# Performance work log

Measured on AMD Instinct MI355X. Metric: run time of the kernel, lower is better.

## Reference

```python
import jax, jax.numpy as jnp
import numpy as np

DIM = 768
HEADS = 12
HEAD_DIM = DIM // HEADS
R = 8            # LoRA rank (cfg.EXPERT_LOW_RANK)
E = 4            # number of routed LoRA experts in proj (cfg.EXPERT_NUM)
LORA_SCALE = 1.0 / R   # lora_alpha(=1) / r
TOPK_T_PCT = 50  # cfg.topk_tempalte (percent)
TOPK_S_PCT = 25  # cfg.topk_search (percent)
B = 4
N_M = 256        # template / memory tokens
N_S = 1024       # search tokens
N = N_M + N_S
MEM = 1280       # cached memory kv length


def setup_inputs() -> dict:
    key = jax.random.key(0)
    ks = jax.random.split(key, 24)
    g = lambda i, shape: jax.random.normal(ks[i], shape, dtype=jnp.float32) * 0.02
    return dict(
        x=jax.random.normal(ks[0], (B, N, DIM), dtype=jnp.float32),
        id_total=jax.random.normal(ks[1], (B, N_M, DIM), dtype=jnp.float32),
        mem_k=jax.random.normal(ks[2], (B, HEADS, MEM, HEAD_DIM), dtype=jnp.float32),
        mem_v=jax.random.normal(ks[3], (B, HEADS, MEM, HEAD_DIM), dtype=jnp.float32),
        W_qkv=g(4, (3 * DIM, DIM)), b_qkv=g(5, (3 * DIM,)),
        qkv_A=g(6, (3, R, DIM)), qkv_B=g(7, (3, DIM, R)),
        W_proj=g(8, (DIM, DIM)), b_proj=g(9, (DIM,)),
        route_W=g(10, (E, DIM)), proj_A=g(11, (E, R, DIM)), proj_B=g(12, (E, DIM, R)),
        W_idk=g(13, (HEADS, DIM)), b_idk=g(14, (HEADS,)),
        idk_A=g(15, (R, DIM)), idk_B=g(16, (HEADS, R)),
        W_idv=g(17, (DIM, DIM)), b_idv=g(18, (DIM,)),
        idv_A=g(19, (R, DIM)), idv_B=g(20, (DIM, R)),
    )


def _lora1(x, W, b, A, Bm):
    # LinearExperts with lora_num=1: softmax over a single route logit == 1.0
    return x @ W.T + b + ((x @ A.T) @ Bm.T) * LORA_SCALE


def _softmax_w_top(att, top):
    # topk values (sorted desc) -> stable exp relative to the max -> normalize -> scatter
    vals, idx = jax.lax.top_k(att, top)
    e = jnp.exp(vals - vals[..., :1])
    e = e / jnp.sum(e, axis=-1, keepdims=True)
    b, h, q, _ = att.shape
    bi = jnp.arange(b)[:, None, None, None]
    hi = jnp.arange(h)[None, :, None, None]
    qi = jnp.arange(q)[None, None, :, None]
    return jnp.zeros_like(att).at[bi, hi, qi, idx].set(e.astype(att.dtype))


def _forward(x, id_total, mem_k, mem_v, W_qkv, b_qkv, qkv_A, qkv_B,
             W_proj, b_proj, route_W, proj_A, proj_B,
             W_idk, b_idk, idk_A, idk_B, W_idv, b_idv, idv_A, idv_B):
    Bb, Nn, C = x.shape
    Nm = id_total.shape[1]
    Ns = Nn - Nm
    H, D = HEADS, C // HEADS
    # MergedLinear qkv: dense + per-group (q,k,v) LoRA
    low = jnp.einsum('bnc,grc->bngr', x, qkv_A)
    lora = (jnp.einsum('bngr,gcr->bngc', low, qkv_B) * LORA_SCALE).reshape(Bb, Nn, 3 * C)
    qkv = (x @ W_qkv.T + b_qkv + lora).reshape(Bb, Nn, 3, H, D).transpose(2, 0, 3, 1, 4)
    q, k, v = qkv[0], qkv[1], qkv[2]          # each (B,H,N,D)
    k_m, v_m, v_s = k[:, :, :Nm], v[:, :, :Nm], v[:, :, Nm:]
    # memory-token ID gating (id_add=True path)
    ID_K = _lora1(id_total, W_idk, b_idk, idk_A, idk_B)   # (B,Nm,H)
    ID_V = _lora1(id_total, W_idv, b_idv, idv_A, idv_B)   # (B,Nm,C)
    k_m_id = k_m * (1.0 + jnp.tanh(ID_K)).transpose(0, 2, 1)[..., None]
    v_m_flat = v_m.transpose(0, 2, 1, 3).reshape(Bb, Nm, C) + ID_V
    v_m_id = v_m_flat.reshape(Bb, Nm, H, D).transpose(0, 2, 1, 3)
    v_add_id = jnp.concatenate([v_m_id, v_s], axis=2)
    q = q * (D ** -0.5)
    q_m, q_s = q[:, :, :Nm], q[:, :, Nm:]
    # template self-attention with topk softmax
    attn_m = q_m @ k_m_id.transpose(0, 1, 3, 2)           # (B,H,Nm,Nm)
    attn_m = _softmax_w_top(attn_m, int(TOPK_T_PCT / 100 * Nm))
    x_m = (attn_m @ v_m_id).transpose(0, 2, 1, 3).reshape(Bb, Nm, C)
    # search attention over [mem_k, k] (k is the ORIGINAL un-gated key, as in torch)
    k_full = jnp.concatenate([mem_k, k], axis=2)
    v_full = jnp.concatenate([mem_v, v_add_id], axis=2)
    attn_s = q_s @ k_full.transpose(0, 1, 3, 2)           # (B,H,Ns,MEM+N)
    attn_s = _softmax_w_top(attn_s, int(TOPK_S_PCT / 100 * k_full.shape[2]))
    x_s = (attn_s @ v_full).transpose(0, 2, 1, 3).reshape(Bb, Ns, C)
    xo = jnp.concatenate([x_m, x_s], axis=1)
    # LinearExperts proj: dense + softmax-routed LoRA experts
    route = jax.nn.softmax((xo @ route_W.T).astype(jnp.float32), axis=-1).astype(xo.dtype)
    low = jnp.einsum('bnc,erc->bner', xo, proj_A)
    up = jnp.einsum('bner,ecr->bnec', low, proj_B)
    out = xo @ W_proj.T + b_proj + jnp.einsum('bne,bnec->bnc', route, up) * LORA_SCALE
    return out, k_m_id, v_m_id


def reference(x, id_total, mem_k, mem_v, W_qkv, b_qkv, qkv_A, qkv_B,
              W_proj, b_proj, route_W, proj_A, proj_B,
              W_idk, b_idk, idk_A, idk_B, W_idv, b_idv, idv_A, idv_B):
    return _forward(x, id_total, mem_k, mem_v, W_qkv, b_qkv, qkv_A, qkv_B,
                    W_proj, b_proj, route_W, proj_A, proj_B,
                    W_idk, b_idk, idk_A, idk_B, W_idv, b_idv, idv_A, idv_B)
```

## Files before the change

### kernel.cpp

```cpp
#include <hip/hip_runtime.h>
#include <cstddef>

#define Bq    4
#define Hh    12
#define Dd    64
#define NNtok 1280
#define DIMc  768
#define KAUG  800
#define NBH   48

typedef __attribute__((ext_vector_type(8))) short bf16x8;
typedef __attribute__((ext_vector_type(4))) float f32x4;

static const size_t OVb   = 0;
static const size_t OXO   = 3932160;
static const size_t OQL   = 7864320;
static const size_t OIDK  = 7987200;
static const size_t OIDV  = 7999488;
static const size_t OLK   = 8785920;
static const size_t OLV   = 8794112;
static const size_t ORD   = 8802304;
static const size_t OPL   = 8822784;
static const size_t OQH   = 8986624;
static const size_t OKFH  = 10952704;
static const size_t OVTH  = 14884864;
static const size_t OKMH  = 18817024;
static const size_t OVMTH = 19210240;
static const size_t OAa   = 19603456;
static const size_t OWa   = 21651456;
static const size_t OWa2  = 22573056;

static const size_t KMID_OFF = 3932160;
static const size_t VMID_OFF = 4718592;

__device__ __forceinline__ unsigned int pk_bf16(float a, float b) {
  unsigned int ua = __float_as_uint(a), ub = __float_as_uint(b);
  ua += 0x7fffu + ((ua >> 16) & 1u);
  ub += 0x7fffu + ((ub >> 16) & 1u);
  return (ua >> 16) | (ub & 0xffff0000u);
}
__device__ __forceinline__ unsigned short bf16_1(float a) {
  unsigned int ua = __float_as_uint(a);
  ua += 0x7fffu + ((ua >> 16) & 1u);
  return (unsigned short)(ua >> 16);
}
__device__ __forceinline__ float bf2f(unsigned int h) {
  return __uint_as_float(h << 16);
}

__global__ __launch_bounds__(256) void prep(
    const float* __restrict__ mem_k, const float* __restrict__ mem_v,
    const float* __restrict__ W_qkv, const float* __restrict__ qkvB,
    const float* __restrict__ W_proj, const float* __restrict__ projB,
    unsigned short* __restrict__ kfh, unsigned short* __restrict__ vth,
    unsigned short* __restrict__ Wa, unsigned short* __restrict__ Wa2)
{
  __shared__ float tl[64][65];
  const int blk = blockIdx.x, t = threadIdx.x;
  if (blk < 1920) {
    size_t idx = ((size_t)blk * 256 + t) * 8;
    int bh = (int)(idx / 81920);
    int r  = (int)(idx % 81920);
    const float* s = mem_k + (size_t)bh * 81920 + r;
    float4 a = *(const float4*)s;
    float4 b = *(const float4*)(s + 4);
    unsigned int* dp = (unsigned int*)(kfh + (size_t)bh * 163840 + r);
    dp[0] = pk_bf16(a.x, a.y); dp[1] = pk_bf16(a.z, a.w);
    dp[2] = pk_bf16(b.x, b.y); dp[3] = pk_bf16(b.z, b.w);
  } else if (blk < 2880) {
    int b2 = blk - 1920;
    int bh = b2 / 20, t0 = (b2 % 20) * 64;
    const float* sb = mem_v + (size_t)bh * 81920 + (size_t)t0 * 64;
#pragma unroll
    for (int p = 0; p < 4; ++p) {
      int flat = p * 256 + t;
      int r = flat >> 4, c4 = (flat & 15) << 2;
      float4 v = *(const float4*)(sb + r * 64 + c4);
      tl[r][c4 + 0] = v.x; tl[r][c4 + 1] = v.y;
      tl[r][c4 + 2] = v.z; tl[r][c4 + 3] = v.w;
    }
    __syncthreads();
    unsigned short* db = vth + (size_t)bh * 163840 + t0;
#pragma unroll
    for (int p = 0; p < 8; ++p) {
      int flat = p * 256 + t;
      int d = flat >> 5, u = flat & 31;
      *(unsigned int*)(db + (size_t)d * 2560 + 2 * u) = pk_bf16(tl[2 * u][d], tl[2 * u + 1][d]);
    }
  } else if (blk < 6480) {
    int idx = (blk - 2880) * 256 + t;
    int row = idx / 400, c = (idx % 400) * 2;
    float a, b;
    if (c < 768) {
      a = W_qkv[(size_t)row * 768 + c]; b = W_qkv[(size_t)row * 768 + c + 1];
    } else {
      int g = row / 768, jj = row % 768;
      int e0 = c - 768, e1 = e0 + 1;
      a = (e0 < 24 && (e0 >> 3) == g) ? qkvB[(size_t)g * 6144 + jj * 8 + (e0 & 7)] * 0.125f : 0.f;
      b = (e1 < 24 && (e1 >> 3) == g) ? qkvB[(size_t)g * 6144 + jj * 8 + (e1 & 7)] * 0.125f : 0.f;
    }
    *(unsigned int*)(Wa + (size_t)row * KAUG + c) = pk_bf16(a, b);
  } else {
    int idx = (blk - 6480) * 256 + t;
    int row = idx / 400, c = (idx % 400) * 2;
    float a, b;
    if (c < 768) {
      a = W_proj[(size_t)row * 768 + c]; b = W_proj[(size_t)row * 768 + c + 1];
    } else {
      int e0 = c - 768, e1 = e0 + 1;
      a = projB[(size_t)(e0 >> 3) * 6144 + row * 8 + (e0 & 7)];
      b = projB[(size_t)(e1 >> 3) * 6144 + row * 8 + (e1 & 7)];
    }
    *(unsigned int*)(Wa2 + (size_t)row * KAUG + c) = pk_bf16(a, b);
  }
}

__global__ __launch_bounds__(256) void dot_small(
    const float* __restrict__ src, const float* __restrict__ mat,
    float* __restrict__ dst, int nout)
{
  int wv = threadIdx.x >> 6, ln = threadIdx.x & 63;
  size_t row = (size_t)blockIdx.x * 4 + wv;
  const float* s = src + row * DIMc;
  for (int o = 0; o < nout; ++o) {
    float p = 0.f;
    const float* m = mat + (size_t)o * DIMc;
    for (int c = ln; c < DIMc; c += 64) p += s[c] * m[c];
    for (int off = 32; off; off >>= 1) p += __shfl_xor(p, off, 64);
    if (ln == 0) dst[row * nout + o] = p;
  }
}

__global__ __launch_bounds__(256) void dot_id(
    const float* __restrict__ id_tot, const float* __restrict__ idkA,
    const float* __restrict__ idvA, float* __restrict__ lowk,
    float* __restrict__ lowv)
{
  int wv = threadIdx.x >> 6, ln = threadIdx.x & 63;
  size_t row = (size_t)blockIdx.x * 4 + wv;
  const float* s = id_tot + row * DIMc;
  for (int o = 0; o < 8; ++o) {
    float p = 0.f, q = 0.f;
    const float* m1 = idkA + (size_t)o * DIMc;
    const float* m2 = idvA + (size_t)o * DIMc;
    for (int c = ln; c < DIMc; c += 64) { p += s[c] * m1[c]; q += s[c] * m2[c]; }
    for (int off = 32; off; off >>= 1) { p += __shfl_xor(p, off, 64); q += __shfl_xor(q, off, 64); }
    if (ln == 0) { lowk[row * 8 + o] = p; lowv[row * 8 + o] = q; }
  }
}

__global__ __launch_bounds__(256) void dot_rp(
    const float* __restrict__ xo, const float* __restrict__ routeW,
    const float* __restrict__ projA, float* __restrict__ rd,
    float* __restrict__ plow)
{
  int wv = threadIdx.x >> 6, ln = threadIdx.x & 63;
  size_t row = (size_t)blockIdx.x * 4 + wv;
  const float* s = xo + row * DIMc;
  float xr[12];
#pragma unroll
  for (int i = 0; i < 12; ++i) xr[i] = s[ln + i * 64];
  for (int o = 0; o < 4; ++o) {
    float p = 0.f;
    const float* m = routeW + (size_t)o * DIMc;
#pragma unroll
    for (int i = 0; i < 12; ++i) p += xr[i] * m[ln + i * 64];
    for (int off = 32; off; off >>= 1) p += __shfl_xor(p, off, 64);
    if (ln == 0) rd[row * 4 + o] = p;
  }
  for (int o = 0; o < 32; ++o) {
    float p = 0.f;
    const float* m = projA + (size_t)o * DIMc;
#pragma unroll
    for (int i = 0; i < 12; ++i) p += xr[i] * m[ln + i * 64];
    for (int off = 32; off; off >>= 1) p += __shfl_xor(p, off, 64);
    if (ln == 0) plow[row * 32 + o] = p;
  }
}

__global__ __launch_bounds__(256) void idv_idk(
    const float* __restrict__ id_tot,
    const float* __restrict__ W_idv, const float* __restrict__ b_idv,
    const float* __restrict__ lowv, const float* __restrict__ idv_B,
    float* __restrict__ IDV,
    const float* __restrict__ W_idk, const float* __restrict__ b_idk,
    const float* __restrict__ lowk, const float* __restrict__ idk_B,
    float* __restrict__ IDK)
{
  __shared__ alignas(16) float As[16][68];
  __shared__ alignas(16) float Bs[16][68];
  const int blk = blockIdx.x, t = threadIdx.x;
  if (blk < 192) {
    const int tx = t & 15, ty = t >> 4;
    const int bn = (blk % 12) * 64, bm = (blk / 12) * 64;
    const int am = t >> 2, ak = (t & 3) << 2;
    float acc[4][4] = {};
    for (int k0 = 0; k0 < 768; k0 += 16) {
      float4 av = *(const float4*)(id_tot + (size_t)(bm + am) * 768 + k0 + ak);
      float4 bv = *(const float4*)(W_idv + (size_t)(bn + am) * 768 + k0 + ak);
      As[ak + 0][am] = av.x; As[ak + 1][am] = av.y; As[ak + 2][am] = av.z; As[ak + 3][am] = av.w;
      Bs[ak + 0][am] = bv.x; Bs[ak + 1][am] = bv.y; Bs[ak + 2][am] = bv.z; Bs[ak + 3][am] = bv.w;
      __syncthreads();
#pragma unroll
      for (int kk = 0; kk < 16; ++kk) {
        float4 a4 = *(const float4*)&As[kk][ty << 2];
        float4 b4 = *(const float4*)&Bs[kk][tx << 2];
        float ar[4] = { a4.x, a4.y, a4.z, a4.w };
        float br[4] = { b4.x, b4.y, b4.z, b4.w };
#pragma unroll
        for (int i = 0; i < 4; ++i)
#pragma unroll
          for (int j = 0; j < 4; ++j) acc[i][j] += ar[i] * br[j];
      }
      __syncthreads();
    }
#pragma unroll
    for (int i = 0; i < 4; ++i) {
      int mg = bm + (ty << 2) + i;
#pragma unroll
      for (int j = 0; j < 4; ++j) {
        int col = bn + (tx << 2) + j;
        float v = acc[i][j] + b_idv[col];
        float lo = 0.f;
#pragma unroll
        for (int r = 0; r < 8; ++r) lo += lowv[(size_t)mg * 8 + r] * idv_B[(size_t)col * 8 + r];
        IDV[(size_t)mg * 768 + col] = v + lo * 0.125f;
      }
    }
  } else {
    int wv = t >> 6, ln = t & 63;
    size_t row = (size_t)(blk - 192) * 4 + wv;
    const float* s = id_tot + row * DIMc;
    for (int h = 0; h < Hh; ++h) {
      float p = 0.f;
      const float* m = W_idk + (size_t)h * DIMc;
      for (int c = ln; c < DIMc; c += 64) p += s[c] * m[c];
      for (int off = 32; off; off >>= 1) p += __shfl_xor(p, off, 64);
      if (ln == 0) {
        float lo = 0.f;
        for (int r = 0; r < 8; ++r) lo += lowk[row * 8 + r] * idk_B[h * 8 + r];
        IDK[row * Hh + h] = 1.f + tanhf(p + b_idk[h] + lo * 0.125f);
      }
    }
  }
}

__global__ __launch_bounds__(256) void fixup_kernel(
    float* __restrict__ vb, const float* __restrict__ IDK,
    const float* __restrict__ IDV, float* __restrict__ kmid,
    float* __restrict__ vmid, unsigned short* __restrict__ kmh)
{
  int e = blockIdx.x * 256 + threadIdx.x;
  int d  = e & 63;
  int r1 = e >> 6;
  int tt = r1 & 255;
  int r2 = r1 >> 8;
  int h  = r2 % Hh;
  int b  = r2 / Hh;
  float km = kmid[e] * IDK[(size_t)(b * 256 + tt) * Hh + h];
  kmid[e] = km;
  kmh[e] = bf16_1(km);
  size_t src = ((size_t)(b * Hh + h) * NNtok + tt) * Dd + d;
  float vv = vb[src] + IDV[(size_t)(b * 256 + tt) * DIMc + h * 64 + d];
  vb[src] = vv;
  vmid[e] = vv;
}

__global__ __launch_bounds__(256) void transpose_post(
    const float* __restrict__ vb, unsigned short* __restrict__ vth,
    unsigned short* __restrict__ vmth)
{
  __shared__ float tl[64][65];
  const int blk = blockIdx.x, t = threadIdx.x;
  int bh, t0, dstCols, colOfs;
  unsigned short* dstp;
  size_t dstBh;
  if (blk < 960) { bh = blk / 20; t0 = (blk % 20) * 64; dstp = vth; dstBh = 163840; dstCols = 2560; colOfs = 1280; }
  else { int b2 = blk - 960; bh = b2 / 4; t0 = (b2 % 4) * 64; dstp = vmth; dstBh = 16384; dstCols = 256; colOfs = 0; }
  const float* sb = vb + (size_t)bh * 81920 + (size_t)t0 * 64;
#pragma unroll
  for (int p = 0; p < 4; ++p) {
    int flat = p * 256 + t;
    int r = flat >> 4, c4 = (flat & 15) << 2;
    float4 v = *(const float4*)(sb + r * 64 + c4);
    tl[r][c4 + 0] = v.x; tl[r][c4 + 1] = v.y;
    tl[r][c4 + 2] = v.z; tl[r][c4 + 3] = v.w;
  }
  __syncthreads();
  unsigned short* db = dstp + (size_t)bh * dstBh + colOfs + t0;
#pragma unroll
  for (int p = 0; p < 8; ++p) {
    int flat = p * 256 + t;
    int d = flat >> 5, u = flat & 31;
    *(unsigned int*)(db + (size_t)d * dstCols + 2 * u) = pk_bf16(tl[2 * u][d], tl[2 * u + 1][d]);
  }
}

__global__ __launch_bounds__(256) void cast_pack(
    const float* __restrict__ mainp, const float* __restrict__ extra,
    unsigned short* __restrict__ dst, int extraN)
{
  int idx = blockIdx.x * 256 + threadIdx.x;
  int row = idx / 100, c8 = (idx % 100) * 8;
  unsigned int w[4];
  if (c8 < 768) {
    const float* s = mainp + (size_t)row * 768 + c8;
    float4 a = *(const float4*)s;
    float4 b = *(const float4*)(s + 4);
    w[0] = pk_bf16(a.x, a.y); w[1] = pk_bf16(a.z, a.w);
    w[2] = pk_bf16(b.x, b.y); w[3] = pk_bf16(b.z, b.w);
  } else {
    float v[8];
#pragma unroll
    for (int j = 0; j < 8; ++j) {
      int e = c8 - 768 + j;
      v[j] = (e < extraN) ? extra[(size_t)row * extraN + e] : 0.f;
    }
    w[0] = pk_bf16(v[0], v[1]); w[1] = pk_bf16(v[2], v[3]);
    w[2] = pk_bf16(v[4], v[5]); w[3] = pk_bf16(v[6], v[7]);
  }
  *(uint4*)(dst + (size_t)row * KAUG + c8) = make_uint4(w[0], w[1], w[2], w[3]);
}

__global__ __launch_bounds__(256) void cast_pack_proj(
    const float* __restrict__ xo, const float* __restrict__ rd,
    const float* __restrict__ plow, unsigned short* __restrict__ dst)
{
  int idx = blockIdx.x * 256 + threadIdx.x;
  int row = idx / 100, c8 = (idx % 100) * 8;
  unsigned int w[4];
  if (c8 < 768) {
    const float* s = xo + (size_t)row * 768 + c8;
    float4 a = *(const float4*)s;
    float4 b = *(const float4*)(s + 4);
    w[0] = pk_bf16(a.x, a.y); w[1] = pk_bf16(a.z, a.w);
    w[2] = pk_bf16(b.x, b.y); w[3] = pk_bf16(b.z, b.w);
  } else {
    float l0 = rd[row * 4 + 0], l1 = rd[row * 4 + 1], l2 = rd[row * 4 + 2], l3 = rd[row * 4 + 3];
    float m = fmaxf(fmaxf(l0, l1), fmaxf(l2, l3));
    float e0 = __expf(l0 - m), e1 = __expf(l1 - m), e2 = __expf(l2 - m), e3 = __expf(l3 - m);
    float inv = 0.125f / (e0 + e1 + e2 + e3);
    float rt[4] = { e0 * inv, e1 * inv, e2 * inv, e3 * inv };
    float v[8];
#pragma unroll
    for (int j = 0; j < 8; ++j) {
      int e = c8 - 768 + j;
      v[j] = (e < 32) ? rt[e >> 3] * plow[(size_t)row * 32 + e] : 0.f;
    }
    w[0] = pk_bf16(v[0], v[1]); w[1] = pk_bf16(v[2], v[3]);
    w[2] = pk_bf16(v[4], v[5]); w[3] = pk_bf16(v[6], v[7]);
  }
  *(uint4*)(dst + (size_t)row * KAUG + c8) = make_uint4(w[0], w[1], w[2], w[3]);
}

__global__ __launch_bounds__(256) void gemm_mfma(
    const unsigned short* __restrict__ A, const unsigned short* __restrict__ W,
    const float* __restrict__ bias, int mode, float* __restrict__ dst,
    unsigned short* __restrict__ qh, float* __restrict__ kmid,
    float* __restrict__ vb, unsigned short* __restrict__ kfh)
{
  const int t = threadIdx.x, w = t >> 6, l = t & 63;
  const int m = l & 15, quad = l >> 4;
  const int bm = blockIdx.y * 128 + (w >> 1) * 64;
  const int bn = blockIdx.x * 128 + (w & 1) * 64;
  f32x4 acc[4][4] = {};
  const unsigned short* Ab = A + (size_t)(bm + m) * KAUG;
  const unsigned short* Wb = W + (size_t)(bn + m) * KAUG;
  for (int kk = 0; kk < KAUG; kk += 32) {
    bf16x8 af[4], bf[4];
#pragma unroll
    for (int i = 0; i < 4; ++i) af[i] = *(const bf16x8*)(Ab + (size_t)i * 16 * KAUG + kk + quad * 8);
#pragma unroll
    for (int j = 0; j < 4; ++j) bf[j] = *(const bf16x8*)(Wb + (size_t)j * 16 * KAUG + kk + quad * 8);
#pragma unroll
    for (int i = 0; i < 4; ++i)
#pragma unroll
      for (int j = 0; j < 4; ++j)
        acc[i][j] = __builtin_amdgcn_mfma_f32_16x16x32_bf16(af[i], bf[j], acc[i][j], 0, 0, 0);
  }

  float bj[4];
#pragma unroll
  for (int j = 0; j < 4; ++j) bj[j] = bias[bn + j * 16 + m];

  if (mode == 2) {
#pragma unroll
    for (int i = 0; i < 4; ++i)
#pragma unroll
      for (int r = 0; r < 4; ++r) {
        int row = bm + i * 16 + quad * 4 + r;
#pragma unroll
        for (int j = 0; j < 4; ++j)
          dst[(size_t)row * 768 + bn + j * 16 + m] = acc[i][j][r] + bj[j];
      }
    return;
  }
  int g = (blockIdx.x * 128) / DIMc;
#pragma unroll
  for (int j = 0; j < 4; ++j) {
    int col = bn + j * 16 + m;
    int jj = col - g * DIMc, hh = jj >> 6, d = jj & 63;
#pragma unroll
    for (int i = 0; i < 4; ++i)
#pragma unroll
      for (int r = 0; r < 4; ++r) {
        int row = bm + i * 16 + quad * 4 + r;
        int bb = row / NNtok, tt = row % NNtok;
        float v = acc[i][j][r] + bj[j];
        if (g == 0) {
          qh[((size_t)(bb * Hh + hh) * NNtok + tt) * Dd + d] = bf16_1(v * 0.125f);
        } else if (g == 1) {
          kfh[((size_t)(bb * Hh + hh) * 2560 + 1280 + tt) * Dd + d] = bf16_1(v);
          if (tt < 256) kmid[((size_t)(bb * Hh + hh) * 256 + tt) * Dd + d] = v;
        } else {
          vb[((size_t)(bb * Hh + hh) * NNtok + tt) * Dd + d] = v;
        }
      }
  }
}

__device__ __forceinline__ void radix_sel(
    unsigned int* hist, int l, int& kk, int& ceq, unsigned int& bin)
{
  unsigned int h0 = hist[4 * l + 0], h1 = hist[4 * l + 1],
               h2 = hist[4 * l + 2], h3 = hist[4 * l + 3];
  unsigned int s3 = h3, s2 = h2 + s3, s1 = h1 + s2, s0 = h0 + s1;
  unsigned int tsum = s0;
#pragma unroll
  for (int off = 1; off < 64; off <<= 1) {
    unsigned int other = __shfl(tsum, l + off, 64);
    tsum += (l + off < 64) ? other : 0u;
  }
  unsigned int T = tsum - s0;
  unsigned int Sv0 = T + s0, Sv1 = T + s1, Sv2 = T + s2, Sv3 = T + s3, Sv4 = T;
  int fb = -1, fkk = 0, fceq = 0;
  unsigned int ukk = (unsigned int)kk;
  if (Sv0 >= ukk && Sv1 < ukk) { fb = 4 * l + 0; fkk = (int)(ukk - Sv1); fceq = (int)(Sv0 - Sv1); }
  if (Sv1 >= ukk && Sv2 < ukk) { fb = 4 * l + 1; fkk = (int)(ukk - Sv2); fceq = (int)(Sv1 - Sv2); }
  if (Sv2 >= ukk && Sv3 < ukk) { fb = 4 * l + 2; fkk = (int)(ukk - Sv3); fceq = (int)(Sv2 - Sv3); }
  if (Sv3 >= ukk && Sv4 < ukk) { fb = 4 * l + 3; fkk = (int)(ukk - Sv4); fceq = (int)(Sv3 - Sv4); }
  unsigned long long mb = __ballot(fb >= 0);
  int src = __ffsll(mb) - 1;
  bin = (unsigned int)__shfl(fb, src, 64);
  kk  = __shfl(fkk, src, 64);
  ceq = __shfl(fceq, src, 64);
}

template<int NK>
__global__ __launch_bounds__(256, 3) void attn_mfma7(
    const unsigned short* __restrict__ qh,
    const unsigned short* __restrict__ kf,
    const unsigned short* __restrict__ vt,
    int TK, int qrow0, float* __restrict__ xo, int nofs)
{
  constexpr int SCP = NK + 8;
  constexpr int W = NK / 128;
  constexpr int NRB = (NK == 256) ? 32 : 128;
  __shared__ alignas(16) unsigned short sc16[8][SCP];
  __shared__ unsigned int hist8[8][256];
  __shared__ float wavemax[4][8];
  __shared__ float rowinv[8];

  const int t = threadIdx.x, w = t >> 6, l = t & 63;
  const int xcd  = (int)blockIdx.x & 7;
  const int slot = (int)blockIdx.x >> 3;
  const int bh   = xcd * (NBH / 8) + slot / NRB;
  const int rb   = slot % NRB;
  const int b = bh / Hh, h = bh % Hh;
  const int qbase = qrow0 + rb * 8;
  const int m = l & 15, quad = l >> 4;

  bf16x8 aq0 = {0,0,0,0,0,0,0,0}, aq1 = {0,0,0,0,0,0,0,0};
  if (m < 8) {
    const unsigned short* qp = qh + ((size_t)bh * NNtok + qbase + m) * Dd + quad * 8;
    aq0 = *(const bf16x8*)qp;
    aq1 = *(const bf16x8*)(qp + 32);
  }
  float mx[4] = { -3.0e38f, -3.0e38f, -3.0e38f, -3.0e38f };
  constexpr int ITA = NK / 64;
  constexpr int GA = (ITA >= 4) ? 4 : ITA;
  const unsigned short* kpA = kf + (size_t)bh * NK * Dd + (size_t)(w * 16 + m) * Dd + quad * 8;
  bf16x8 kbuf[2][GA][2];
#pragma unroll
  for (int i = 0; i < GA; ++i) {
    kbuf[0][i][0] = *(const bf16x8*)(kpA + (size_t)i * 64 * Dd);
    kbuf[0][i][1] = *(const bf16x8*)(kpA + (size_t)i * 64 * Dd + 32);
  }
  int ab = 0;
  for (int g0 = 0; g0 < ITA; g0 += GA) {
    if (g0 + GA < ITA) {
#pragma unroll
      for (int i = 0; i < GA; ++i) {
        kbuf[1 - ab][i][0] = *(const bf16x8*)(kpA + (size_t)(g0 + GA + i) * 64 * Dd);
        kbuf[1 - ab][i][1] = *(const bf16x8*)(kpA + (size_t)(g0 + GA + i) * 64 * Dd + 32);
      }
    }
#pragma unroll
    for (int i = 0; i < GA; ++i) {
      int n0 = w * 16 + (g0 + i) * 64;
      f32x4 acc = {0.f, 0.f, 0.f, 0.f};
      acc = __builtin_amdgcn_mfma_f32_16x16x32_bf16(aq0, kbuf[ab][i][0], acc, 0, 0, 0);
      acc = __builtin_amdgcn_mfma_f32_16x16x32_bf16(aq1, kbuf[ab][i][1], acc, 0, 0, 0);
      if (quad < 2) {
#pragma unroll
        for (int r = 0; r < 4; ++r) {
          float v = acc[r];
          mx[r] = fmaxf(mx[r], v);
          sc16[quad * 4 + r][n0 + m] = bf16_1(v);
        }
      }
    }
    ab ^= 1;
  }
#pragma unroll
  for (int off = 1; off < 16; off <<= 1)
#pragma unroll
    for (int r = 0; r < 4; ++r) mx[r] = fmaxf(mx[r], __shfl_xor(mx[r], off, 64));
  if (l == 0) {
#pragma unroll
    for (int r = 0; r < 4; ++r) wavemax[w][r] = mx[r];
  }
  if (l == 16) {
#pragma unroll
    for (int r = 0; r < 4; ++r) wavemax[w][4 + r] = mx[r];
  }
  __syncthreads();

  const int r0i = w * 2, r1i = w * 2 + 1;
  unsigned int* sp0 = (unsigned int*)&sc16[r0i][0];
  unsigned int* sp1 = (unsigned int*)&sc16[r1i][0];
  unsigned int* h0 = hist8[r0i];
  unsigned int* h1 = hist8[r1i];
#pragma unroll
  for (int z = 0; z < 4; ++z) { h0[l + z * 64] = 0u; h1[l + z * 64] = 0u; }
  unsigned int kw0[W], kw1[W];
#pragma unroll
  for (int j = 0; j < W; ++j) {
    unsigned int v0 = sp0[j * 64 + l];
    unsigned int v1 = sp1[j * 64 + l];
    v0 = v0 ^ (((v0 >> 15) & 0x00010001u) * 0x7fffu + 0x80008000u);
    v1 = v1 ^ (((v1 >> 15) & 0x00010001u) * 0x7fffu + 0x80008000u);
    kw0[j] = v0; kw1[j] = v1;
    atomicAdd(&h0[(v0 >> 8) & 255u], 1u);
    atomicAdd(&h0[v0 >> 24], 1u);
    atomicAdd(&h1[(v1 >> 8) & 255u], 1u);
    atomicAdd(&h1[v1 >> 24], 1u);
  }
  int kk0 = TK, kk1 = TK;
  int ceq0s, ceq1s;
  unsigned int bin0, bin1;
  radix_sel(h0, l, kk0, ceq0s, bin0);
  radix_sel(h1, l, kk1, ceq1s, bin1);
  const unsigned int pf0 = bin0 << 8, pf1 = bin1 << 8;
  (void)ceq0s; (void)ceq1s;

  auto finish = [&](unsigned int* kwp, unsigned int prefix, int kk, int row,
                    unsigned int* sp) {
    unsigned int* hist = hist8[row];
#pragma unroll
    for (int z = 0; z < 4; ++z) hist[l + z * 64] = 0u;
    const unsigned int pfx8 = prefix >> 8;
#pragma unroll
    for (int j = 0; j < W; ++j) {
      unsigned int k2 = kwp[j];
      unsigned int lo = k2 & 0xFFFFu, hi = k2 >> 16;
      if ((lo >> 8) == pfx8) atomicAdd(&hist[lo & 255u], 1u);
      if ((hi >> 8) == pfx8) atomicAdd(&hist[hi & 255u], 1u);
    }
    unsigned int b2;
    int ceq = 0;
    radix_sel(hist, l, kk, ceq, b2);
    const unsigned int Tkey = prefix | b2;
    const int need = kk;
    if (need < ceq) {
      int seen = 0;
      unsigned long long below = (1ull << l) - 1ull;
#pragma unroll
      for (int j = 0; j < W; ++j) {
        unsigned int k2 = kwp[j];
        bool eq0 = ((k2 & 0xFFFFu) == Tkey);
        bool eq1 = ((k2 >> 16) == Tkey);
        unsigned long long m0 = __ballot(eq0), m1 = __ballot(eq1);
        int bfr = __popcll(m0 & below) + __popcll(m1 & below);
        if (eq0 && (seen + bfr) >= need) kwp[j] &= 0xFFFF0000u;
        if (eq1 && (seen + bfr + (eq0 ? 1 : 0)) >= need) kwp[j] &= 0x0000FFFFu;
        seen += __popcll(m0) + __popcll(m1);
      }
    }
    float rm = fmaxf(fmaxf(wavemax[0][row], wavemax[1][row]),
                     fmaxf(wavemax[2][row], wavemax[3][row]));
    float sum = 0.f;
#pragma unroll
    for (int j = 0; j < W; ++j) {
      unsigned int k2 = kwp[j];
      unsigned int lo = k2 & 0xFFFFu, hi = k2 >> 16;
      unsigned int mm = ((~k2 >> 15) & 0x00010001u) * 0x7fffu + 0x80008000u;
      unsigned int o2 = k2 ^ mm;
      float v0 = bf2f(o2 & 0xFFFFu);
      float v1 = bf2f(o2 >> 16);
      float w0 = (lo >= Tkey) ? __expf(v0 - rm) : 0.f;
      float w1 = (hi >= Tkey) ? __expf(v1 - rm) : 0.f;
      sp[j * 64 + l] = pk_bf16(w0, w1);
      sum += w0 + w1;
    }
#pragma unroll
    for (int off = 32; off; off >>= 1) sum += __shfl_xor(sum, off, 64);
    if (l == 0) rowinv[row] = 1.f / sum;
  };
  finish(kw0, pf0, kk0, r0i, sp0);
  finish(kw1, pf1, kk1, r1i, sp1);
  __syncthreads();

  constexpr int ITD = NK / 32;
  constexpr int GD = (ITD >= 4) ? 4 : ITD;
  const unsigned short* vrow = vt + (size_t)bh * Dd * NK + (size_t)(w * 16 + m) * NK + quad * 8;
  f32x4 o = {0.f, 0.f, 0.f, 0.f};
  const bf16x8 zz = {0,0,0,0,0,0,0,0};
  bf16x8 vbuf[2][GD], wbuf[2][GD];
#pragma unroll
  for (int i = 0; i < GD; ++i) {
    vbuf[0][i] = *(const bf16x8*)(vrow + i * 32);
    wbuf[0][i] = (m < 8) ? *(const bf16x8*)&sc16[m][i * 32 + quad * 8] : zz;
  }
  int db = 0;
  for (int g0 = 0; g0 < ITD; g0 += GD) {
    if (g0 + GD < ITD) {
#pragma unroll
      for (int i = 0; i < GD; ++i) {
        vbuf[1 - db][i] = *(const bf16x8*)(vrow + (g0 + GD + i) * 32);
        wbuf[1 - db][i] = (m < 8) ? *(const bf16x8*)&sc16[m][(g0 + GD + i) * 32 + quad * 8] : zz;
      }
    }
#pragma unroll
    for (int i = 0; i < GD; ++i)
      o = __builtin_amdgcn_mfma_f32_16x16x32_bf16(wbuf[db][i], vbuf[db][i], o, 0, 0, 0);
    db ^= 1;
  }
  if (quad < 2) {
#pragma unroll
    for (int r = 0; r < 4; ++r) {
      int row = quad * 4 + r;
      int n = nofs + rb * 8 + row;
      xo[((size_t)b * NNtok + n) * DIMc + h * 64 + w * 16 + m] = o[r] * rowinv[row];
    }
  }
}

extern "C" void kernel_launch(void* const* d_in, const int* in_sizes, int n_in,
                              void* d_out, int out_size, void* d_ws, size_t ws_size,
                              hipStream_t stream)
{
  const float* x       = (const float*)d_in[0];
  const float* id_tot  = (const float*)d_in[1];
  const float* mem_k   = (const float*)d_in[2];
  const float* mem_v   = (const float*)d_in[3];
  const float* W_qkv   = (const float*)d_in[4];
  const float* b_qkv   = (const float*)d_in[5];
  const float* qkv_A   = (const float*)d_in[6];
  const float* qkv_B   = (const float*)d_in[7];
  const float* W_proj  = (const float*)d_in[8];
  const float* b_proj  = (const float*)d_in[9];
  const float* route_W = (const float*)d_in[10];
  const float* proj_A  = (const float*)d_in[11];
  const float* proj_B  = (const float*)d_in[12];
  const float* W_idk   = (const float*)d_in[13];
  const float* b_idk   = (const float*)d_in[14];
  const float* idk_A   = (const float*)d_in[15];
  const float* idk_B   = (const float*)d_in[16];
  const float* W_idv   = (const float*)d_in[17];
  const float* b_idv   = (const float*)d_in[18];
  const float* idv_A   = (const float*)d_in[19];
  const float* idv_B   = (const float*)d_in[20];

  float* ws   = (float*)d_ws;
  float* vb   = ws + OVb;
  float* xo   = ws + OXO;
  float* qlow = ws + OQL;
  float* IDK  = ws + OIDK;
  float* IDV  = ws + OIDV;
  float* lowk = ws + OLK;
  float* lowv = ws + OLV;
  float* rd   = ws + ORD;
  float* plow = ws + OPL;
  unsigned short* qh   = (unsigned short*)(ws + OQH);
  unsigned short* kfh  = (unsigned short*)(ws + OKFH);
  unsigned short* vth  = (unsigned short*)(ws + OVTH);
  unsigned short* kmh  = (unsigned short*)(ws + OKMH);
  unsigned short* vmth = (unsigned short*)(ws + OVMTH);
  unsigned short* Aa   = (unsigned short*)(ws + OAa);
  unsigned short* Wa   = (unsigned short*)(ws + OWa);
  unsigned short* Wa2  = (unsigned short*)(ws + OWa2);

  float* out  = (float*)d_out;
  float* kmid = out + KMID_OFF;
  float* vmid = out + VMID_OFF;

  prep<<<7680, 256, 0, stream>>>(mem_k, mem_v, W_qkv, qkv_B, W_proj, proj_B,
                                 kfh, vth, Wa, Wa2);

  dot_small<<<1280, 256, 0, stream>>>(x, qkv_A, qlow, 24);
  dot_id<<<256, 256, 0, stream>>>(id_tot, idk_A, idv_A, lowk, lowv);

  cast_pack<<<2000, 256, 0, stream>>>(x, qlow, Aa, 24);
  gemm_mfma<<<dim3(18, 40), 256, 0, stream>>>(Aa, Wa, b_qkv, 0, nullptr,
                                              qh, kmid, vb, kfh);
  idv_idk<<<448, 256, 0, stream>>>(id_tot, W_idv, b_idv, lowv, idv_B, IDV,
                                   W_idk, b_idk, lowk, idk_B, IDK);
  fixup_kernel<<<3072, 256, 0, stream>>>(vb, IDK, IDV, kmid, vmid, kmh);

  transpose_post<<<1152, 256, 0, stream>>>(vb, vth, vmth);

  attn_mfma7<256><<<1536, 256, 0, stream>>>(qh, kmh, vmth, 128, 0, xo, 0);
  attn_mfma7<2560><<<6144, 256, 0, stream>>>(qh, kfh, vth, 640, 256, xo, 256);

  dot_rp<<<1280, 256, 0, stream>>>(xo, route_W, proj_A, rd, plow);
  cast_pack_proj<<<2000, 256, 0, stream>>>(xo, rd, plow, Aa);
  gemm_mfma<<<dim3(6, 40), 256, 0, stream>>>(Aa, Wa2, b_proj, 2, out,
                                             nullptr, nullptr, nullptr, nullptr);
}
```

Measured before the change: 914.9 us.

## Shrink attention LDS footprint via XOR swizzle and aliased histogram for higher occupancy

Removes the padded score rows, separate histogram, wavemax and rowinv shared arrays. Scores are stored with an XOR swizzle instead of padding to avoid bank conflicts. For large NK the radix histogram now reuses each row's score buffer while keys sit in registers, and the row max comes from the encoded keys via a wave reduction. Launch bounds rise from 3 to 4 blocks per CU, trading two extra barriers and more aliasing complexity for higher occupancy.

After: 1.064 ms. 16.2% more time.

```diff
diff --git a/kernel.cpp b/kernel.cpp
--- a/kernel.cpp
+++ b/kernel.cpp
@@ -447,19 +447,15 @@
 }
 
 template<int NK>
-__global__ __launch_bounds__(256, 3) void attn_mfma7(
+__global__ __launch_bounds__(256, 4) void attn_mfma7(
     const unsigned short* __restrict__ qh,
     const unsigned short* __restrict__ kf,
     const unsigned short* __restrict__ vt,
     int TK, int qrow0, float* __restrict__ xo, int nofs)
 {
-  constexpr int SCP = NK + 8;
   constexpr int W = NK / 128;
   constexpr int NRB = (NK == 256) ? 32 : 128;
-  __shared__ alignas(16) unsigned short sc16[8][SCP];
-  __shared__ unsigned int hist8[8][256];
-  __shared__ float wavemax[4][8];
-  __shared__ float rowinv[8];
+  __shared__ alignas(16) unsigned short sc16[8 * NK];
 
   const int t = threadIdx.x, w = t >> 6, l = t & 63;
   const int xcd  = (int)blockIdx.x & 7;
@@ -476,7 +472,6 @@
     aq0 = *(const bf16x8*)qp;
     aq1 = *(const bf16x8*)(qp + 32);
   }
-  float mx[4] = { -3.0e38f, -3.0e38f, -3.0e38f, -3.0e38f };
   constexpr int ITA = NK / 64;
   constexpr int GA = (ITA >= 4) ? 4 : ITA;
   const unsigned short* kpA = kf + (size_t)bh * NK * Dd + (size_t)(w * 16 + m) * Dd + quad * 8;
@@ -504,73 +499,87 @@
       if (quad < 2) {
 #pragma unroll
         for (int r = 0; r < 4; ++r) {
-          float v = acc[r];
-          mx[r] = fmaxf(mx[r], v);
-          sc16[quad * 4 + r][n0 + m] = bf16_1(v);
+          int row = quad * 4 + r;
+          int s = n0 + m;
+          int dw = (s >> 1) ^ (row << 2);
+          sc16[row * NK + dw * 2 + (s & 1)] = bf16_1(acc[r]);
         }
       }
     }
     ab ^= 1;
   }
-#pragma unroll
-  for (int off = 1; off < 16; off <<= 1)
-#pragma unroll
-    for (int r = 0; r < 4; ++r) mx[r] = fmaxf(mx[r], __shfl_xor(mx[r], off, 64));
-  if (l == 0) {
-#pragma unroll
-    for (int r = 0; r < 4; ++r) wavemax[w][r] = mx[r];
-  }
-  if (l == 16) {
-#pragma unroll
-    for (int r = 0; r < 4; ++r) wavemax[w][4 + r] = mx[r];
-  }
   __syncthreads();
 
   const int r0i = w * 2, r1i = w * 2 + 1;
-  unsigned int* sp0 = (unsigned int*)&sc16[r0i][0];
-  unsigned int* sp1 = (unsigned int*)&sc16[r1i][0];
-  unsigned int* h0 = hist8[r0i];
-  unsigned int* h1 = hist8[r1i];
-#pragma unroll
-  for (int z = 0; z < 4; ++z) { h0[l + z * 64] = 0u; h1[l + z * 64] = 0u; }
+  unsigned int* sp0 = (unsigned int*)&sc16[r0i * NK];
+  unsigned int* sp1 = (unsigned int*)&sc16[r1i * NK];
+  const int sw0 = r0i << 2, sw1 = r1i << 2;
   unsigned int kw0[W], kw1[W];
+  unsigned int km0 = 0u, km1 = 0u;
 #pragma unroll
   for (int j = 0; j < W; ++j) {
-    unsigned int v0 = sp0[j * 64 + l];
-    unsigned int v1 = sp1[j * 64 + l];
+    unsigned int v0 = sp0[(j * 64 + l) ^ sw0];
+    unsigned int v1 = sp1[(j * 64 + l) ^ sw1];
     v0 = v0 ^ (((v0 >> 15) & 0x00010001u) * 0x7fffu + 0x80008000u);
     v1 = v1 ^ (((v1 >> 15) & 0x00010001u) * 0x7fffu + 0x80008000u);
     kw0[j] = v0; kw1[j] = v1;
-    atomicAdd(&h0[(v0 >> 8) & 255u], 1u);
-    atomicAdd(&h0[v0 >> 24], 1u);
-    atomicAdd(&h1[(v1 >> 8) & 255u], 1u);
-    atomicAdd(&h1[v1 >> 24], 1u);
+    unsigned int a0 = v0 & 0xFFFFu, b0 = v0 >> 16;
+    unsigned int a1 = v1 & 0xFFFFu, b1 = v1 >> 16;
+    km0 = max(km0, max(a0, b0));
+    km1 = max(km1, max(a1, b1));
+  }
+#pragma unroll
+  for (int off = 1; off < 64; off <<= 1) {
+    km0 = max(km0, (unsigned int)__shfl_xor((int)km0, off, 64));
+    km1 = max(km1, (unsigned int)__shfl_xor((int)km1, off, 64));
+  }
+  unsigned int ti0 = (km0 & 0x8000u) ? (km0 ^ 0x8000u) : (km0 ^ 0xFFFFu);
+  unsigned int ti1 = (km1 & 0x8000u) ? (km1 ^ 0x8000u) : (km1 ^ 0xFFFFu);
+  const float rm0 = bf2f(ti0 & 0xFFFFu);
+  const float rm1 = bf2f(ti1 & 0xFFFFu);
+
+  unsigned int *h0, *h1;
+  if constexpr (NK == 256) {
+    __shared__ unsigned int hsep[2048];
+    h0 = &hsep[r0i * 256];
+    h1 = &hsep[r1i * 256];
+  } else {
+    h0 = sp0;
+    h1 = sp1;
+    __builtin_amdgcn_sched_barrier(0);
+  }
+#pragma unroll
+  for (int z = 0; z < 4; ++z) { h0[l + z * 64] = 0u; h1[l + z * 64] = 0u; }
+#pragma unroll
+  for (int j = 0; j < W; ++j) {
+    atomicAdd(&h0[(kw0[j] >> 8) & 255u], 1u);
+    atomicAdd(&h0[kw0[j] >> 24], 1u);
+    atomicAdd(&h1[(kw1[j] >> 8) & 255u], 1u);
+    atomicAdd(&h1[kw1[j] >> 24], 1u);
   }
   int kk0 = TK, kk1 = TK;
-  int ceq0s, ceq1s;
+  int ce0s, ce1s;
   unsigned int bin0, bin1;
-  radix_sel(h0, l, kk0, ceq0s, bin0);
-  radix_sel(h1, l, kk1, ceq1s, bin1);
-  const unsigned int pf0 = bin0 << 8, pf1 = bin1 << 8;
-  (void)ceq0s; (void)ceq1s;
-
-  auto finish = [&](unsigned int* kwp, unsigned int prefix, int kk, int row,
-                    unsigned int* sp) {
-    unsigned int* hist = hist8[row];
+  radix_sel(h0, l, kk0, ce0s, bin0);
+  radix_sel(h1, l, kk1, ce1s, bin1);
+  (void)ce0s; (void)ce1s;
+
+  auto finish = [&](unsigned int* kwp, unsigned int bin, int kk,
+                    unsigned int* hist, unsigned int* sp, int sw,
+                    float rm) -> float {
 #pragma unroll
     for (int z = 0; z < 4; ++z) hist[l + z * 64] = 0u;
-    const unsigned int pfx8 = prefix >> 8;
 #pragma unroll
     for (int j = 0; j < W; ++j) {
       unsigned int k2 = kwp[j];
       unsigned int lo = k2 & 0xFFFFu, hi = k2 >> 16;
-      if ((lo >> 8) == pfx8) atomicAdd(&hist[lo & 255u], 1u);
-      if ((hi >> 8) == pfx8) atomicAdd(&hist[hi & 255u], 1u);
+      if ((lo >> 8) == bin) atomicAdd(&hist[lo & 255u], 1u);
+      if ((hi >> 8) == bin) atomicAdd(&hist[hi & 255u], 1u);
     }
     unsigned int b2;
     int ceq = 0;
     radix_sel(hist, l, kk, ceq, b2);
-    const unsigned int Tkey = prefix | b2;
+    const unsigned int Tkey = (bin << 8) | b2;
     const int need = kk;
     if (need < ceq) {
       int seen = 0;
@@ -587,8 +596,6 @@
         seen += __popcll(m0) + __popcll(m1);
       }
     }
-    float rm = fmaxf(fmaxf(wavemax[0][row], wavemax[1][row]),
-                     fmaxf(wavemax[2][row], wavemax[3][row]));
     float sum = 0.f;
 #pragma unroll
     for (int j = 0; j < W; ++j) {
@@ -600,15 +607,15 @@
       float v1 = bf2f(o2 >> 16);
       float w0 = (lo >= Tkey) ? __expf(v0 - rm) : 0.f;
       float w1 = (hi >= Tkey) ? __expf(v1 - rm) : 0.f;
-      sp[j * 64 + l] = pk_bf16(w0, w1);
+      sp[(j * 64 + l) ^ sw] = pk_bf16(w0, w1);
       sum += w0 + w1;
     }
 #pragma unroll
     for (int off = 32; off; off >>= 1) sum += __shfl_xor(sum, off, 64);
-    if (l == 0) rowinv[row] = 1.f / sum;
+    return 1.f / sum;
   };
-  finish(kw0, pf0, kk0, r0i, sp0);
-  finish(kw1, pf1, kk1, r1i, sp1);
+  float inv0 = finish(kw0, bin0, kk0, h0, sp0, sw0, rm0);
+  float inv1 = finish(kw1, bin1, kk1, h1, sp1, sw1, rm1);
   __syncthreads();
 
   constexpr int ITD = NK / 32;
@@ -616,11 +623,14 @@
   const unsigned short* vrow = vt + (size_t)bh * Dd * NK + (size_t)(w * 16 + m) * NK + quad * 8;
   f32x4 o = {0.f, 0.f, 0.f, 0.f};
   const bf16x8 zz = {0,0,0,0,0,0,0,0};
+  const int wsw = (m & 7) << 2;
   bf16x8 vbuf[2][GD], wbuf[2][GD];
 #pragma unroll
   for (int i = 0; i < GD; ++i) {
     vbuf[0][i] = *(const bf16x8*)(vrow + i * 32);
-    wbuf[0][i] = (m < 8) ? *(const bf16x8*)&sc16[m][i * 32 + quad * 8] : zz;
+    wbuf[0][i] = (m < 8)
+        ? *(const bf16x8*)&sc16[(m & 7) * NK + (((i * 16 + quad * 4) ^ wsw) << 1)]
+        : zz;
   }
   int db = 0;
   for (int g0 = 0; g0 < ITD; g0 += GD) {
@@ -628,7 +638,9 @@
 #pragma unroll
       for (int i = 0; i < GD; ++i) {
         vbuf[1 - db][i] = *(const bf16x8*)(vrow + (g0 + GD + i) * 32);
-        wbuf[1 - db][i] = (m < 8) ? *(const bf16x8*)&sc16[m][(g0 + GD + i) * 32 + quad * 8] : zz;
+        wbuf[1 - db][i] = (m < 8)
+            ? *(const bf16x8*)&sc16[(m & 7) * NK + ((((g0 + GD + i) * 16 + quad * 4) ^ wsw) << 1)]
+            : zz;
       }
     }
 #pragma unroll
@@ -636,12 +648,17 @@
       o = __builtin_amdgcn_mfma_f32_16x16x32_bf16(wbuf[db][i], vbuf[db][i], o, 0, 0, 0);
     db ^= 1;
   }
+
+  __syncthreads();
+  float* invp = (float*)&sc16[0];
+  if (l == 0) { invp[r0i] = inv0; invp[r1i] = inv1; }
+  __syncthreads();
   if (quad < 2) {
 #pragma unroll
     for (int r = 0; r < 4; ++r) {
       int row = quad * 4 + r;
       int n = nofs + rb * 8 + row;
-      xo[((size_t)b * NNtok + n) * DIMc + h * 64 + w * 16 + m] = o[r] * rowinv[row];
+      xo[((size_t)b * NNtok + n) * DIMc + h * 64 + w * 16 + m] = o[r] * invp[row];
     }
   }
 }
```
